# Performance work log

Measured on AMD Instinct MI355X. Metric: run time of the kernel, lower is better.

Reference implementation:

```python
import jax, jax.numpy as jnp
import numpy as np

IN_FEATURES = 256
OUT_FEATURES = 256
GRID_SIZE = 5
SPLINE_ORDER = 3
GRID_RANGE = (-1.0, 1.0)
LN_EPS = 1e-5


def _make_grid():
    h = (GRID_RANGE[1] - GRID_RANGE[0]) / GRID_SIZE
    n_knots = GRID_SIZE + 2 * SPLINE_ORDER + 1  # 12
    return jnp.linspace(GRID_RANGE[0] - h * SPLINE_ORDER,
                        GRID_RANGE[1] + h * SPLINE_ORDER,
                        n_knots, dtype=jnp.float32)


def setup_inputs() -> dict:
    key = jax.random.key(0)
    k1, k2, k3 = jax.random.split(key, 3)
    N = 65536
    # kaiming_uniform_(nonlinearity='linear'): bound = sqrt(3/fan_in)
    b1 = np.sqrt(3.0 / IN_FEATURES)
    fan_sp = IN_FEATURES * (GRID_SIZE + SPLINE_ORDER)
    b2 = np.sqrt(3.0 / fan_sp)
    return {
        "x": jax.random.normal(k1, (N, IN_FEATURES), dtype=jnp.float32),
        "grid": _make_grid(),
        "base_weight": jax.random.uniform(k2, (OUT_FEATURES, IN_FEATURES), jnp.float32, -b1, b1),
        "spline_weight": jax.random.uniform(k3, (OUT_FEATURES, IN_FEATURES, GRID_SIZE + SPLINE_ORDER), jnp.float32, -b2, b2),
        "ln_gamma": jnp.ones((OUT_FEATURES,), jnp.float32),
        "ln_beta": jnp.zeros((OUT_FEATURES,), jnp.float32),
        "prelu_a": jnp.full((1,), 0.25, jnp.float32),
    }


def reference(x, grid, base_weight, spline_weight, ln_gamma, ln_beta, prelu_a):
    # base branch: exact GELU then linear (matches nn.GELU() + F.linear)
    base_out = jnp.einsum('ni,oi->no', jax.nn.gelu(x, approximate=False), base_weight)

    # Cox-de Boor B-spline basis recursion. grid is identical per feature in
    # the original ([in, 12] expand of a 1D linspace) so we broadcast the 1D grid.
    xu = x[:, :, None]                                   # [N, in, 1]
    bases = ((xu >= grid[:-1]) & (xu < grid[1:])).astype(x.dtype)  # [N, in, 11]
    for k in range(1, SPLINE_ORDER + 1):
        left = grid[:-(k + 1)]
        right = grid[k:-1]
        delta = jnp.where(right == left, jnp.ones_like(right), right - left)
        bases = ((xu - left) / delta * bases[:, :, :-1]
                 + (grid[k + 1:] - xu) / (grid[k + 1:] - grid[1:-k]) * bases[:, :, 1:])
    # bases: [N, in, grid_size + spline_order]

    spline_out = jnp.einsum('nig,oig->no', bases, spline_weight)

    y = base_out + spline_out
    mu = jnp.mean(y, axis=-1, keepdims=True)
    var = jnp.mean(jnp.square(y - mu), axis=-1, keepdims=True)
    y = (y - mu) * jax.lax.rsqrt(var + LN_EPS) * ln_gamma + ln_beta
    # PReLU with a single shared slope (nn.PReLU default)
    return jnp.where(y >= 0, y, prelu_a[0] * y)
```

## Files before the change

### kernel.cpp

```cpp
#include <hip/hip_runtime.h>
#include <hip/hip_bf16.h>
#include <math.h>
#include <stdint.h>

typedef __attribute__((ext_vector_type(8))) short short8;
typedef __attribute__((ext_vector_type(4))) float f32x4;

#define BM 256
#define NKT 36
#define A_BYTES (BM * 128)
#define LDS_TOTAL (4 * A_BYTES)

__device__ __forceinline__ unsigned short f2bf(float f) {
    __bf16 h = (__bf16)f;
    return __builtin_bit_cast(unsigned short, h);
}

__device__ __forceinline__ float gelu_exact(float x) {
    return 0.5f * x * (1.0f + erff(x * 0.7071067811865475f));
}

__device__ __forceinline__ int swz(int row, int u) {
    return row * 128 + ((u ^ (row & 7)) << 4);
}

__global__ void kan_prep_w(const float* __restrict__ bw, const float* __restrict__ sw,
                           unsigned short* __restrict__ Wf) {
    int U = blockIdx.x * 256 + threadIdx.x;
    if (U >= NKT * 2048) return;
    int kt = U >> 11, rem = U & 2047;
    int wcq = rem >> 9, rem2 = rem & 511;
    int i = rem2 >> 6;
    int lane = rem2 & 63;
    int o = wcq * 64 + (i & 3) * 16 + (lane & 15);
    int k0 = kt * 64 + ((i >> 2) * 4 + (lane >> 4)) * 8;
    unsigned short pk[8];
#pragma unroll
    for (int e = 0; e < 8; ++e) {
        int kk = k0 + e;
        float v = (kk < 256) ? bw[o * 256 + kk] : sw[o * 2048 + (kk - 256)];
        pk[e] = f2bf(v);
    }
    *(short8*)(Wf + (size_t)U * 8) = *(short8*)pk;
}

__device__ __forceinline__ short8 spline_row(float xv) {
    float xi = (xv + 2.2f) * 2.5f;
    float fi = floorf(xi);
    float tt = xi - fi;
    float s1 = 1.0f - tt;
    float t2 = tt * tt, t3 = t2 * tt;
    float w0 = s1 * s1 * s1 * (1.0f / 6.0f);
    float w1 = 0.5f * t3 - t2 + (2.0f / 3.0f);
    float w2 = -0.5f * t3 + 0.5f * t2 + 0.5f * tt + (1.0f / 6.0f);
    float w3 = t3 * (1.0f / 6.0f);
    uint64_t Wp = (uint64_t)f2bf(w0) | ((uint64_t)f2bf(w1) << 16)
                | ((uint64_t)f2bf(w2) << 32) | ((uint64_t)f2bf(w3) << 48);
    int b = 16 * ((int)fi - 3);
    uint64_t L = (b >= 0 && b < 64) ? (Wp << b)
               : ((b < 0 && b > -64) ? (Wp >> (-b)) : 0ull);
    uint64_t H = (b >= 64 && b < 128) ? (Wp << (b - 64))
               : ((b > 0 && b < 64) ? (Wp >> (64 - b)) : 0ull);
    union { uint64_t q[2]; short8 v; } rr;
    rr.q[0] = L; rr.q[1] = H;
    return rr.v;
}

__global__ __launch_bounds__(512)
void kan_fused(
    const float* __restrict__ X, const unsigned short* __restrict__ Wf,
    const float* __restrict__ gamma, const float* __restrict__ beta,
    const float* __restrict__ prelu_a, float* __restrict__ OUT)
{
    extern __shared__ __align__(16) unsigned char lds[];

    const int t = threadIdx.x;
    const int row0 = blockIdx.x * BM;
    const int wid = t >> 6, lane = t & 63;
    const int wr = wid >> 2, wc = wid & 3;
    const int lcol = lane & 15, q = lane >> 4;
    const int srow = t >> 3, scol = t & 7;

    f32x4 acc[8][4];
#pragma unroll
    for (int m = 0; m < 8; ++m)
#pragma unroll
        for (int n = 0; n < 4; ++n) acc[m][n] = (f32x4){0.f, 0.f, 0.f, 0.f};

    const unsigned short* wlane = Wf + ((size_t)wc * 512 + lane) * 8;
    short8 wv[8];

    auto w_load = [&](int kt) {
        const unsigned short* wsrc = wlane + (size_t)kt * 2048 * 8;
#pragma unroll
        for (int i = 0; i < 8; ++i)
            wv[i] = *(const short8*)(wsrc + i * 512);
    };
    auto gelu_stage = [&](int kt, unsigned char* D) {
#pragma unroll
        for (int rep = 0; rep < 4; ++rep) {
            const float* xp = X + (size_t)(row0 + srow + rep * 64) * 256 + kt * 64 + scol * 8;
            float4 v0 = *(const float4*)xp;
            float4 v1 = *(const float4*)(xp + 4);
            float vv[8] = {v0.x, v0.y, v0.z, v0.w, v1.x, v1.y, v1.z, v1.w};
            unsigned short pk[8];
#pragma unroll
            for (int jj = 0; jj < 8; ++jj) pk[jj] = f2bf(gelu_exact(vv[jj]));
            *(short8*)(D + swz(srow + rep * 64, scol)) = *(short8*)pk;
        }
    };
    auto spline_stage = [&](float (&xs)[4], unsigned char* D) {
#pragma unroll
        for (int rep = 0; rep < 4; ++rep)
            *(short8*)(D + swz(srow + rep * 64, scol)) = spline_row(xs[rep]);
    };
    auto mfma_tile = [&](unsigned char* B) {
        __builtin_amdgcn_s_setprio(1);
#pragma unroll
        for (int kh = 0; kh < 2; ++kh) {
            short8 af[8];
#pragma unroll
            for (int m = 0; m < 8; ++m)
                af[m] = *(const short8*)(B + swz(wr * 128 + m * 16 + lcol, kh * 4 + q));
#pragma unroll
            for (int m = 0; m < 8; ++m)
#pragma unroll
                for (int n = 0; n < 4; ++n)
                    acc[m][n] = __builtin_amdgcn_mfma_f32_16x16x32_bf16(
                        af[m], wv[kh * 4 + n], acc[m][n], 0, 0, 0);
        }
        __builtin_amdgcn_s_setprio(0);
    };

    w_load(0);
    gelu_stage(0, lds);
    gelu_stage(1, lds + A_BYTES);
    asm volatile("s_waitcnt lgkmcnt(0)\n\ts_barrier" ::: "memory");

    for (int j = 0; j < NKT / 2; ++j) {
        const int ka = 2 * j, kb = ka + 1;
        unsigned char* Ba = lds + (ka & 3) * A_BYTES;
        unsigned char* Bb = lds + (kb & 3) * A_BYTES;
        unsigned char* Sa = lds + ((ka + 2) & 3) * A_BYTES;
        unsigned char* Sb = lds + ((ka + 3) & 3) * A_BYTES;
        const bool stg = (ka + 2 < NKT);
        const bool gA = (ka + 2 < 4), gB = (ka + 3 < 4);

        float xsA[4], xsB[4];
        if (stg && !gA) {
            const int ibA = (ka + 2 - 4) * 8;
#pragma unroll
            for (int rep = 0; rep < 4; ++rep)
                xsA[rep] = X[(size_t)(row0 + srow + rep * 64) * 256 + ibA + scol];
        }
        if (stg && !gB) {
            const int ibB = (ka + 3 - 4) * 8;
#pragma unroll
            for (int rep = 0; rep < 4; ++rep)
                xsB[rep] = X[(size_t)(row0 + srow + rep * 64) * 256 + ibB + scol];
        }

        if ((wid & 1) == 0) {
            mfma_tile(Ba);
            w_load(kb);
            if (stg) { if (gA) gelu_stage(ka + 2, Sa); else spline_stage(xsA, Sa); }
            mfma_tile(Bb);
            if (stg) w_load(ka + 2);
            if (stg) { if (gB) gelu_stage(ka + 3, Sb); else spline_stage(xsB, Sb); }
        } else {
            if (stg) { if (gA) gelu_stage(ka + 2, Sa); else spline_stage(xsA, Sa); }
            mfma_tile(Ba);
            w_load(kb);
            if (stg) { if (gB) gelu_stage(ka + 3, Sb); else spline_stage(xsB, Sb); }
            mfma_tile(Bb);
            if (stg) w_load(ka + 2);
        }

        asm volatile("s_waitcnt lgkmcnt(0)\n\ts_barrier" ::: "memory");
    }

    float* stats = (float*)lds;
#pragma unroll
    for (int m = 0; m < 8; ++m) {
#pragma unroll
        for (int r = 0; r < 4; ++r) {
            float s = 0.f, s2 = 0.f;
#pragma unroll
            for (int n = 0; n < 4; ++n) { float v = acc[m][n][r]; s += v; s2 += v * v; }
#pragma unroll
            for (int msk = 1; msk < 16; msk <<= 1) {
                s  += __shfl_xor(s,  msk, 64);
                s2 += __shfl_xor(s2, msk, 64);
            }
            if ((lane & 15) == ((m * 4 + r) & 15)) {
                int row = wr * 128 + m * 16 + q * 4 + r;
                stats[row * 8 + wc]     = s;
                stats[row * 8 + 4 + wc] = s2;
            }
        }
    }
    __syncthreads();

    const float apr = prelu_a[0];
    float gv[4], bv[4];
#pragma unroll
    for (int n = 0; n < 4; ++n) {
        int col = wc * 64 + n * 16 + lcol;
        gv[n] = gamma[col]; bv[n] = beta[col];
    }
#pragma unroll
    for (int m = 0; m < 8; ++m) {
#pragma unroll
        for (int r = 0; r < 4; ++r) {
            int row = wr * 128 + m * 16 + q * 4 + r;
            f32x4 sv = *(const f32x4*)(stats + row * 8);
            f32x4 qv = *(const f32x4*)(stats + row * 8 + 4);
            float mu  = (sv[0] + sv[1] + sv[2] + sv[3]) * (1.0f / 256.0f);
            float ex2 = (qv[0] + qv[1] + qv[2] + qv[3]) * (1.0f / 256.0f);
            float rs = rsqrtf(ex2 - mu * mu + 1e-5f);
            float* op = OUT + (size_t)(row0 + row) * 256;
#pragma unroll
            for (int n = 0; n < 4; ++n) {
                int col = wc * 64 + n * 16 + lcol;
                float y = (acc[m][n][r] - mu) * rs * gv[n] + bv[n];
                op[col] = (y >= 0.f) ? y : apr * y;
            }
        }
    }
}

extern "C" void kernel_launch(void* const* d_in, const int* in_sizes, int n_in,
                              void* d_out, int out_size, void* d_ws, size_t ws_size,
                              hipStream_t stream) {
    const float* x  = (const float*)d_in[0];
    const float* bw = (const float*)d_in[2];
    const float* sw = (const float*)d_in[3];
    const float* g  = (const float*)d_in[4];
    const float* be = (const float*)d_in[5];
    const float* pa = (const float*)d_in[6];
    float* out = (float*)d_out;
    unsigned short* Wf = (unsigned short*)d_ws;

    hipFuncSetAttribute((const void*)kan_fused,
                        hipFuncAttributeMaxDynamicSharedMemorySize, LDS_TOTAL);

    const int Nrows = in_sizes[0] / 256;
    kan_prep_w<<<(NKT * 2048 + 255) / 256, 256, 0, stream>>>(bw, sw, Wf);
    kan_fused<<<Nrows / BM, 512, LDS_TOTAL, stream>>>(x, Wf, g, be, pa, out);
}
```

Before: 125.0 us.

## Switch GEMM to 32x32x16 bf16 MFMA tiles with matching weight layout

Replaces the 16x16x32 bf16 MFMA instruction with the 32x32x16 variant. The per-wave accumulator becomes 4x2 tiles of 16 floats, and the LDS A-fragment reads, the weight pre-pack layout and the LayerNorm epilogue row/column mapping are rewritten to match. Each wave issues fewer, larger MFMAs and fewer LDS fragment loads per k-step, which should raise matrix-core throughput per LDS byte. The epilogue needs a wider 32-lane shuffle reduction, and the new output mapping may change store coalescing.

Result: no change. 125.2 us (+0.1%).

```diff
diff --git a/kernel.cpp b/kernel.cpp
--- a/kernel.cpp
+++ b/kernel.cpp
@@ -5,6 +5,7 @@
 
 typedef __attribute__((ext_vector_type(8))) short short8;
 typedef __attribute__((ext_vector_type(4))) float f32x4;
+typedef __attribute__((ext_vector_type(16))) float f32x16;
 
 #define BM 256
 #define NKT 36
@@ -32,8 +33,8 @@
     int wcq = rem >> 9, rem2 = rem & 511;
     int i = rem2 >> 6;
     int lane = rem2 & 63;
-    int o = wcq * 64 + (i & 3) * 16 + (lane & 15);
-    int k0 = kt * 64 + ((i >> 2) * 4 + (lane >> 4)) * 8;
+    int o = wcq * 64 + (i & 1) * 32 + (lane & 31);
+    int k0 = kt * 64 + (i >> 1) * 16 + (lane >> 5) * 8;
     unsigned short pk[8];
 #pragma unroll
     for (int e = 0; e < 8; ++e) {
@@ -78,14 +79,16 @@
     const int row0 = blockIdx.x * BM;
     const int wid = t >> 6, lane = t & 63;
     const int wr = wid >> 2, wc = wid & 3;
-    const int lcol = lane & 15, q = lane >> 4;
+    const int l31 = lane & 31, l5 = lane >> 5;
     const int srow = t >> 3, scol = t & 7;
 
-    f32x4 acc[8][4];
-#pragma unroll
-    for (int m = 0; m < 8; ++m)
-#pragma unroll
-        for (int n = 0; n < 4; ++n) acc[m][n] = (f32x4){0.f, 0.f, 0.f, 0.f};
+    f32x16 acc[4][2];
+#pragma unroll
+    for (int mt = 0; mt < 4; ++mt)
+#pragma unroll
+        for (int nt = 0; nt < 2; ++nt)
+#pragma unroll
+            for (int e = 0; e < 16; ++e) acc[mt][nt][e] = 0.f;
 
     const unsigned short* wlane = Wf + ((size_t)wc * 512 + lane) * 8;
     short8 wv[8];
@@ -117,17 +120,17 @@
     auto mfma_tile = [&](unsigned char* B) {
         __builtin_amdgcn_s_setprio(1);
 #pragma unroll
-        for (int kh = 0; kh < 2; ++kh) {
-            short8 af[8];
-#pragma unroll
-            for (int m = 0; m < 8; ++m)
-                af[m] = *(const short8*)(B + swz(wr * 128 + m * 16 + lcol, kh * 4 + q));
-#pragma unroll
-            for (int m = 0; m < 8; ++m)
-#pragma unroll
-                for (int n = 0; n < 4; ++n)
-                    acc[m][n] = __builtin_amdgcn_mfma_f32_16x16x32_bf16(
-                        af[m], wv[kh * 4 + n], acc[m][n], 0, 0, 0);
+        for (int ks = 0; ks < 4; ++ks) {
+            short8 af[4];
+#pragma unroll
+            for (int mt = 0; mt < 4; ++mt)
+                af[mt] = *(const short8*)(B + swz(wr * 128 + mt * 32 + l31, ks * 2 + l5));
+#pragma unroll
+            for (int mt = 0; mt < 4; ++mt)
+#pragma unroll
+                for (int nt = 0; nt < 2; ++nt)
+                    acc[mt][nt] = __builtin_amdgcn_mfma_f32_32x32x16_bf16(
+                        af[mt], wv[ks * 2 + nt], acc[mt][nt], 0, 0, 0);
         }
         __builtin_amdgcn_s_setprio(0);
     };
@@ -181,19 +184,19 @@
 
     float* stats = (float*)lds;
 #pragma unroll
-    for (int m = 0; m < 8; ++m) {
-#pragma unroll
-        for (int r = 0; r < 4; ++r) {
-            float s = 0.f, s2 = 0.f;
-#pragma unroll
-            for (int n = 0; n < 4; ++n) { float v = acc[m][n][r]; s += v; s2 += v * v; }
-#pragma unroll
-            for (int msk = 1; msk < 16; msk <<= 1) {
+    for (int mt = 0; mt < 4; ++mt) {
+#pragma unroll
+        for (int r = 0; r < 16; ++r) {
+            float v0 = acc[mt][0][r], v1 = acc[mt][1][r];
+            float s = v0 + v1, s2 = v0 * v0 + v1 * v1;
+#pragma unroll
+            for (int msk = 1; msk < 32; msk <<= 1) {
                 s  += __shfl_xor(s,  msk, 64);
                 s2 += __shfl_xor(s2, msk, 64);
             }
-            if ((lane & 15) == ((m * 4 + r) & 15)) {
-                int row = wr * 128 + m * 16 + q * 4 + r;
+            int row_local = (r & 3) + 8 * (r >> 2) + 4 * l5;
+            if (l31 == row_local) {
+                int row = wr * 128 + mt * 32 + row_local;
                 stats[row * 8 + wc]     = s;
                 stats[row * 8 + 4 + wc] = s2;
             }
@@ -202,17 +205,17 @@
     __syncthreads();
 
     const float apr = prelu_a[0];
-    float gv[4], bv[4];
-#pragma unroll
-    for (int n = 0; n < 4; ++n) {
-        int col = wc * 64 + n * 16 + lcol;
-        gv[n] = gamma[col]; bv[n] = beta[col];
-    }
-#pragma unroll
-    for (int m = 0; m < 8; ++m) {
-#pragma unroll
-        for (int r = 0; r < 4; ++r) {
-            int row = wr * 128 + m * 16 + q * 4 + r;
+    float gv[2], bv[2];
+#pragma unroll
+    for (int nt = 0; nt < 2; ++nt) {
+        int col = wc * 64 + nt * 32 + l31;
+        gv[nt] = gamma[col]; bv[nt] = beta[col];
+    }
+#pragma unroll
+    for (int mt = 0; mt < 4; ++mt) {
+#pragma unroll
+        for (int r = 0; r < 16; ++r) {
+            int row = wr * 128 + mt * 32 + (r & 3) + 8 * (r >> 2) + 4 * l5;
             f32x4 sv = *(const f32x4*)(stats + row * 8);
             f32x4 qv = *(const f32x4*)(stats + row * 8 + 4);
             float mu  = (sv[0] + sv[1] + sv[2] + sv[3]) * (1.0f / 256.0f);
@@ -220,9 +223,9 @@
             float rs = rsqrtf(ex2 - mu * mu + 1e-5f);
             float* op = OUT + (size_t)(row0 + row) * 256;
 #pragma unroll
-            for (int n = 0; n < 4; ++n) {
-                int col = wc * 64 + n * 16 + lcol;
-                float y = (acc[m][n][r] - mu) * rs * gv[n] + bv[n];
+            for (int nt = 0; nt < 2; ++nt) {
+                int col = wc * 64 + nt * 32 + l31;
+                float y = (acc[mt][nt][r] - mu) * rs * gv[nt] + bv[nt];
                 op[col] = (y >= 0.f) ? y : apr * y;
             }
         }
```
